# Optimization experiments

Measured on AMD Instinct MI355X. Metric: run time of the kernel, lower is better.

The kernel has to match this reference:

```python
import jax, jax.numpy as jnp
import numpy as np

N_NODES = 100_000
N_EDGES = 1_600_000
N_GRAPHS = 512
D_NODE = 128
H = 128
L_EXTRA = 2  # model_layer - 1


def _bn(x, g, b, eps=1e-5):
    # BatchNorm1d, training-mode math (biased batch variance), eval dropout = identity
    mu = jnp.mean(x, axis=0)
    var = jnp.var(x, axis=0)
    return g * (x - mu) * jax.lax.rsqrt(var + eps) + b


def _gin_conv(x, src, dst, W1, b1, bng, bnb, W2, b2):
    # GINConv (eps=0): mlp(x + sum_{j->i} x_j); mlp = Lin -> BN -> ReLU -> Lin
    agg = jax.ops.segment_sum(x[src], dst, num_segments=x.shape[0])
    h = x + agg
    h = jax.nn.relu(_bn(h @ W1 + b1, bng, bnb))
    return h @ W2 + b2


def setup_inputs():
    key = jax.random.key(0)
    ks = jax.random.split(key, 24)
    s = 0.05
    d = {}
    d["x"] = jax.random.normal(ks[0], (N_NODES, D_NODE), dtype=jnp.float32)
    d["edge_index"] = jax.random.randint(ks[1], (2, N_EDGES), 0, N_NODES, dtype=jnp.int32)
    d["batch"] = jnp.sort(jax.random.randint(ks[2], (N_NODES,), 0, N_GRAPHS, dtype=jnp.int32))
    d["vn_emb"] = jax.random.normal(ks[3], (1, H)) * s
    # conv1 MLP: Linear(D_NODE, 2H) -> BN -> ReLU -> Linear(2H, H)
    d["c1_W1"] = jax.random.normal(ks[4], (D_NODE, 2 * H)) * s
    d["c1_b1"] = jnp.zeros((2 * H,))
    d["c1_bng"] = jnp.ones((2 * H,))
    d["c1_bnb"] = jnp.zeros((2 * H,))
    d["c1_W2"] = jax.random.normal(ks[5], (2 * H, H)) * s
    d["c1_b2"] = jnp.zeros((H,))
    d["bn1_g"] = jnp.ones((H,))
    d["bn1_b"] = jnp.zeros((H,))
    # stacked extra GIN layers (model_layer - 1)
    d["cW1"] = jax.random.normal(ks[6], (L_EXTRA, H, 2 * H)) * s
    d["cb1"] = jnp.zeros((L_EXTRA, 2 * H))
    d["cbng"] = jnp.ones((L_EXTRA, 2 * H))
    d["cbnb"] = jnp.zeros((L_EXTRA, 2 * H))
    d["cW2"] = jax.random.normal(ks[7], (L_EXTRA, 2 * H, H)) * s
    d["cb2"] = jnp.zeros((L_EXTRA, H))
    d["bns_g"] = jnp.ones((L_EXTRA, H))
    d["bns_b"] = jnp.zeros((L_EXTRA, H))
    # virtual node MLP: Lin(H,2H)->BN->ReLU->Lin(2H,H)->BN->ReLU->Dropout
    d["vW1"] = jax.random.normal(ks[8], (H, 2 * H)) * s
    d["vb1"] = jnp.zeros((2 * H,))
    d["vbn1_g"] = jnp.ones((2 * H,))
    d["vbn1_b"] = jnp.zeros((2 * H,))
    d["vW2"] = jax.random.normal(ks[9], (2 * H, H)) * s
    d["vb2"] = jnp.zeros((H,))
    d["vbn2_g"] = jnp.ones((H,))
    d["vbn2_b"] = jnp.zeros((H,))
    return d


def reference(x, edge_index, batch, vn_emb, c1_W1, c1_b1, c1_bng, c1_bnb, c1_W2, c1_b2,
              bn1_g, bn1_b, cW1, cb1, cbng, cbnb, cW2, cb2, bns_g, bns_b,
              vW1, vb1, vbn1_g, vbn1_b, vW2, vb2, vbn2_g, vbn2_b):
    src, dst = edge_index[0], edge_index[1]
    # virtual node feature per graph: Embedding(1, H) indexed with zeros
    vfeat = jnp.broadcast_to(vn_emb[0], (N_GRAPHS, H))
    # layer 1: dropout is identity in eval mode
    post = jax.nn.relu(_bn(_gin_conv(x, src, dst, c1_W1, c1_b1, c1_bng, c1_bnb, c1_W2, c1_b2), bn1_g, bn1_b))
    for i in range(L_EXTRA):
        post = post + vfeat[batch]                       # virtual-node broadcast
        post = _bn(_gin_conv(post, src, dst, cW1[i], cb1[i], cbng[i], cbnb[i], cW2[i], cb2[i]), bns_g[i], bns_b[i])
        if i < L_EXTRA - 1:
            post = jax.nn.relu(post)
            pooled = jax.ops.segment_sum(post, batch, num_segments=N_GRAPHS)  # GlobalAddPool
            z = pooled + vfeat
            z = jax.nn.relu(_bn(z @ vW1 + vb1, vbn1_g, vbn1_b))
            vfeat = jax.nn.relu(_bn(z @ vW2 + vb2, vbn2_g, vbn2_b))
    # readout: global mean pool over nodes per graph
    counts = jax.ops.segment_sum(jnp.ones((x.shape[0],), post.dtype), batch, num_segments=N_GRAPHS)
    out = jax.ops.segment_sum(post, batch, num_segments=N_GRAPHS) / jnp.maximum(counts, 1.0)[:, None]
    return out
```

## Files before the change

kernel.cpp:

```cpp
#include <hip/hip_runtime.h>

#define NN 100000
#define NE 1600000
#define NG 512
#define DH 128
#define DH2 256
#define SCB 98
#define NSTRIPE 32

typedef __attribute__((ext_vector_type(8))) _Float16 h8;
typedef __attribute__((ext_vector_type(2))) _Float16 h2;
typedef __attribute__((ext_vector_type(4))) float f4;

static inline size_t align256(size_t x) { return (x + 255) & ~size_t(255); }

__global__ __launch_bounds__(256) void countslot_k(const int* __restrict__ ei,
                                                   int* __restrict__ cursor,
                                                   int* __restrict__ slot) {
    int i = blockIdx.x * blockDim.x + threadIdx.x;
    int stride = gridDim.x * blockDim.x;
    for (int e = i; e < NE; e += stride)
        slot[e] = atomicAdd(&cursor[ei[NE + e]], 1);
}

__global__ __launch_bounds__(256) void place_k(const int* __restrict__ ei,
                                               const int* __restrict__ rowptr,
                                               const int* __restrict__ slot,
                                               int* __restrict__ esrc) {
    int i = blockIdx.x * blockDim.x + threadIdx.x;
    int stride = gridDim.x * blockDim.x;
    for (int e = i; e < NE; e += stride)
        esrc[rowptr[ei[NE + e]] + slot[e]] = ei[e];
}

__global__ void gbound_k(const int* __restrict__ batch, int* __restrict__ gcnt) {
    int g = blockIdx.x * blockDim.x + threadIdx.x;
    if (g >= NG) return;
    int lo = 0, hi = NN;
    while (lo < hi) { int m = (lo + hi) >> 1; if (batch[m] < g) lo = m + 1; else hi = m; }
    int b0 = lo;
    lo = 0; hi = NN;
    int g1 = g + 1;
    while (lo < hi) { int m = (lo + hi) >> 1; if (batch[m] < g1) lo = m + 1; else hi = m; }
    gcnt[g] = lo - b0;
}

__global__ __launch_bounds__(256) void scan1_k(const int* __restrict__ deg,
                                               int* __restrict__ part) {
    int i0 = blockIdx.x * 1024 + threadIdx.x * 4;
    int s = 0;
    if (i0 < NN) {
        int4 v = *(const int4*)(deg + i0);
        s = v.x + v.y + v.z + v.w;
    }
#pragma unroll
    for (int o = 1; o < 64; o <<= 1) s += __shfl_xor(s, o);
    __shared__ int ws[4];
    if ((threadIdx.x & 63) == 0) ws[threadIdx.x >> 6] = s;
    __syncthreads();
    if (threadIdx.x == 0) part[blockIdx.x] = ws[0] + ws[1] + ws[2] + ws[3];
}

__global__ void scan2_k(int* __restrict__ part, int* __restrict__ rowptr) {
    if (threadIdx.x == 0) {
        int run = 0;
        for (int i = 0; i < SCB; i++) { int v = part[i]; part[i] = run; run += v; }
        rowptr[NN] = run;
    }
}

__global__ __launch_bounds__(256) void scan3_k(const int* __restrict__ deg,
                                               const int* __restrict__ part,
                                               int* __restrict__ rowptr) {
    int t = threadIdx.x;
    int i0 = blockIdx.x * 1024 + t * 4;
    int4 v = {0, 0, 0, 0};
    if (i0 < NN) v = *(const int4*)(deg + i0);
    int s = v.x + v.y + v.z + v.w;
    __shared__ int sc[256];
    sc[t] = s;
    __syncthreads();
    for (int o = 1; o < 256; o <<= 1) {
        int add = (t >= o) ? sc[t - o] : 0;
        __syncthreads();
        sc[t] += add;
        __syncthreads();
    }
    int excl = (t ? sc[t - 1] : 0) + part[blockIdx.x];
    if (i0 < NN) {
        int4 r;
        r.x = excl;
        r.y = excl + v.x;
        r.z = excl + v.x + v.y;
        r.w = excl + v.x + v.y + v.z;
        *(int4*)(rowptr + i0) = r;
    }
}

__global__ void castx_k(const float* __restrict__ x, _Float16* __restrict__ xh) {
    int i = blockIdx.x * blockDim.x + threadIdx.x;
    if (i >= NN * 16) return;
    const float4* s = (const float4*)x + i * 2;
    float4 p = s[0], q = s[1];
    h8 h = {(_Float16)p.x, (_Float16)p.y, (_Float16)p.z, (_Float16)p.w,
            (_Float16)q.x, (_Float16)q.y, (_Float16)q.z, (_Float16)q.w};
    ((h8*)xh)[i] = h;
}

__global__ void vinit_k(const float* __restrict__ emb, _Float16* __restrict__ vfeat) {
    int i = blockIdx.x * blockDim.x + threadIdx.x;
    if (i < NG * DH) vfeat[i] = (_Float16)emb[i & (DH - 1)];
}

__global__ void zin_k(const float* __restrict__ pooled, const _Float16* __restrict__ vf,
                      _Float16* __restrict__ zb) {
    int i = blockIdx.x * blockDim.x + threadIdx.x;
    if (i < NG * DH) zb[i] = (_Float16)(pooled[i] + (float)vf[i]);
}

__global__ void addvn_k(_Float16* __restrict__ x, const _Float16* __restrict__ vfeat,
                        const int* __restrict__ batch) {
    int i = blockIdx.x * blockDim.x + threadIdx.x;
    if (i >= NN * 16) return;
    int row = i >> 4;
    int bg = batch[row];
    h8 u = ((h8*)x)[i];
    h8 v = ((const h8*)vfeat)[bg * 16 + (i & 15)];
    h8 o;
#pragma unroll
    for (int e = 0; e < 8; e++) o[e] = (_Float16)((float)u[e] + (float)v[e]);
    ((h8*)x)[i] = o;
}

__global__ void finalout_k(const float* __restrict__ pooled2, const int* __restrict__ gcnt,
                           float* __restrict__ outp) {
    int i = blockIdx.x * blockDim.x + threadIdx.x;
    if (i >= NG * DH) return;
    float cnt = (float)gcnt[i >> 7];
    outp[i] = pooled2[i] / fmaxf(cnt, 1.0f);
}

__global__ void bnfin_k(const float* __restrict__ csum, const float* __restrict__ csq,
                        const float* __restrict__ g, const float* __restrict__ b,
                        float* __restrict__ scale, float* __restrict__ shift,
                        int NC, int M) {
    int col = threadIdx.x;
    if (col >= NC) return;
    float s = 0.f, q = 0.f;
    for (int st = 0; st < NSTRIPE; st++) { s += csum[st * NC + col]; q += csq[st * NC + col]; }
    float invM = 1.0f / (float)M;
    float mean = s * invM;
    float var = q * invM - mean * mean;
    float sc = g[col] * rsqrtf(var + 1e-5f);
    scale[col] = sc;
    shift[col] = b[col] - mean * sc;
}

struct WPack {
    const float* w[8];
    _Float16* wt[8];
    int K[8];
    int N[8];
};
__global__ void wtrans_k(WPack p) {
    int id = blockIdx.z;
    const float* W = p.w[id];
    _Float16* Wt = p.wt[id];
    int K = p.K[id], N = p.N[id];
    int n0 = blockIdx.x * 32, k0 = blockIdx.y * 32;
    if (n0 >= N || k0 >= K) return;
    __shared__ float t[32][33];
    int tx = threadIdx.x & 31, ty = threadIdx.x >> 5;
    for (int i = 0; i < 32; i += 8)
        t[ty + i][tx] = W[(size_t)(k0 + ty + i) * N + n0 + tx];
    __syncthreads();
    for (int i = 0; i < 32; i += 8)
        Wt[(size_t)(n0 + ty + i) * K + k0 + tx] = (_Float16)t[tx][ty + i];
}

__global__ __launch_bounds__(256) void agg_k(const _Float16* __restrict__ xin,
                                             const int* __restrict__ rowptr,
                                             const int* __restrict__ esrc,
                                             _Float16* __restrict__ out) {
    int wave = threadIdx.x >> 6, lane = threadIdx.x & 63;
    int node = blockIdx.x * 4 + wave;
    if (node >= NN) return;
    const h2* xr = (const h2*)xin;
    h2 self = xr[(size_t)node * 64 + lane];
    float a0 = (float)self.x, a1 = (float)self.y;
    int beg = rowptr[node], end = rowptr[node + 1];
    int j = beg;
    for (; j + 7 < end; j += 8) {
        int s0 = esrc[j],     s1 = esrc[j + 1], s2 = esrc[j + 2], s3 = esrc[j + 3];
        int s4 = esrc[j + 4], s5 = esrc[j + 5], s6 = esrc[j + 6], s7 = esrc[j + 7];
        h2 u0 = xr[(size_t)s0 * 64 + lane];
        h2 u1 = xr[(size_t)s1 * 64 + lane];
        h2 u2 = xr[(size_t)s2 * 64 + lane];
        h2 u3 = xr[(size_t)s3 * 64 + lane];
        h2 u4 = xr[(size_t)s4 * 64 + lane];
        h2 u5 = xr[(size_t)s5 * 64 + lane];
        h2 u6 = xr[(size_t)s6 * 64 + lane];
        h2 u7 = xr[(size_t)s7 * 64 + lane];
        a0 += ((float)u0.x + (float)u1.x) + ((float)u2.x + (float)u3.x)
            + ((float)u4.x + (float)u5.x) + ((float)u6.x + (float)u7.x);
        a1 += ((float)u0.y + (float)u1.y) + ((float)u2.y + (float)u3.y)
            + ((float)u4.y + (float)u5.y) + ((float)u6.y + (float)u7.y);
    }
    for (; j < end; j++) {
        h2 u = xr[(size_t)esrc[j] * 64 + lane];
        a0 += (float)u.x; a1 += (float)u.y;
    }
    h2 o; o.x = (_Float16)a0; o.y = (_Float16)a1;
    ((h2*)out)[(size_t)node * 64 + lane] = o;
}

template <int K, int NCF>
__global__ __launch_bounds__(256, 2) void mgemm_k(
        const _Float16* __restrict__ A, const _Float16* __restrict__ Wt,
        const float* __restrict__ bias, _Float16* __restrict__ C,
        float* __restrict__ csum, float* __restrict__ csq, int M,
        const float* __restrict__ bnsc, const float* __restrict__ bnsh) {
    constexpr int BK = 128;
    constexpr int LDA = BK + 8;
    __shared__ __align__(16) _Float16 As[128 * LDA];
    const int tid = threadIdx.x;
    const int lane = tid & 63;
    const int wave = tid >> 6;
    const int wr = wave & 1, wc = wave >> 1;
    const int lm = lane & 15, lq = lane >> 4;
    const int mB = blockIdx.x * 128;
    const int n0 = blockIdx.y * 128 + wc * 64;

    f4 acc[4][4];
#pragma unroll
    for (int i = 0; i < 4; i++)
#pragma unroll
        for (int j = 0; j < 4; j++) acc[i][j] = (f4){0.f, 0.f, 0.f, 0.f};

    const int sr = tid >> 4;
    const int sc = (tid & 15) * 8;

    for (int kc = 0; kc < K; kc += BK) {
        if (kc) __syncthreads();
        float bscv[8], bshv[8];
        if (bnsc) {
            float4 s0 = *(const float4*)&bnsc[kc + sc];
            float4 s1 = *(const float4*)&bnsc[kc + sc + 4];
            float4 t0 = *(const float4*)&bnsh[kc + sc];
            float4 t1 = *(const float4*)&bnsh[kc + sc + 4];
            bscv[0] = s0.x; bscv[1] = s0.y; bscv[2] = s0.z; bscv[3] = s0.w;
            bscv[4] = s1.x; bscv[5] = s1.y; bscv[6] = s1.z; bscv[7] = s1.w;
            bshv[0] = t0.x; bshv[1] = t0.y; bshv[2] = t0.z; bshv[3] = t0.w;
            bshv[4] = t1.x; bshv[5] = t1.y; bshv[6] = t1.z; bshv[7] = t1.w;
        }
#pragma unroll
        for (int rr = 0; rr < 128; rr += 16) {
            int gr = mB + rr + sr; if (gr >= M) gr = M - 1;
            h8 h = *(const h8*)&A[(size_t)gr * K + kc + sc];
            if (bnsc) {
#pragma unroll
                for (int e = 0; e < 8; e++)
                    h[e] = (_Float16)fmaxf((float)h[e] * bscv[e] + bshv[e], 0.f);
            }
            *(h8*)&As[(rr + sr) * LDA + sc] = h;
        }
        __syncthreads();
#pragma unroll
        for (int ks = 0; ks < BK / 32; ks++) {
            h8 af[4], bf[4];
#pragma unroll
            for (int t = 0; t < 4; t++) {
                af[t] = *(const h8*)&As[(wr * 64 + t * 16 + lm) * LDA + ks * 32 + lq * 8];
                bf[t] = *(const h8*)&Wt[(size_t)(n0 + t * 16 + lm) * K + kc + ks * 32 + lq * 8];
            }
#pragma unroll
            for (int i = 0; i < 4; i++)
#pragma unroll
                for (int j = 0; j < 4; j++)
                    acc[i][j] = __builtin_amdgcn_mfma_f32_16x16x32_f16(af[i], bf[j], acc[i][j], 0, 0, 0);
        }
    }

    float bv[4];
#pragma unroll
    for (int j = 0; j < 4; j++) bv[j] = bias[n0 + j * 16 + lm];
    float ls[4] = {0, 0, 0, 0}, lsq[4] = {0, 0, 0, 0};
    __syncthreads();
    _Float16* Cs = As;
#pragma unroll
    for (int i = 0; i < 4; i++) {
        int row = wr * 64 + i * 16 + lq * 4;
        bool rv[4];
#pragma unroll
        for (int r = 0; r < 4; r++) rv[r] = (mB + row + r) < M;
#pragma unroll
        for (int j = 0; j < 4; j++) {
#pragma unroll
            for (int r = 0; r < 4; r++) {
                float v = acc[i][j][r] + bv[j];
                Cs[(row + r) * LDA + wc * 64 + j * 16 + lm] = (_Float16)v;
                if (rv[r]) { ls[j] += v; lsq[j] += v * v; }
            }
        }
    }
    const int stripe = blockIdx.x & (NSTRIPE - 1);
#pragma unroll
    for (int j = 0; j < 4; j++) {
        float s = ls[j], q = lsq[j];
        s += __shfl_xor(s, 16); s += __shfl_xor(s, 32);
        q += __shfl_xor(q, 16); q += __shfl_xor(q, 32);
        if (lq == 0) {
            atomicAdd(&csum[stripe * NCF + n0 + j * 16 + lm], s);
            atomicAdd(&csq[stripe * NCF + n0 + j * 16 + lm], q);
        }
    }
    __syncthreads();
    const int trow = tid >> 4;
    const int tcol = (tid & 15) * 8;
    const int cb = blockIdx.y * 128;
#pragma unroll
    for (int p = 0; p < 8; p++) {
        int row = p * 16 + trow;
        int grow = mB + row;
        if (grow < M) {
            h8 v = *(const h8*)&Cs[row * LDA + tcol];
            *(h8*)&C[(size_t)grow * NCF + cb + tcol] = v;
        }
    }
}

__global__ void bnrelu_k(const _Float16* __restrict__ in, _Float16* __restrict__ out,
                         const float* __restrict__ scale, const float* __restrict__ shift,
                         const _Float16* __restrict__ vfeat, const int* __restrict__ batch,
                         int M) {
    constexpr int PER = 16;
    int tid = blockIdx.x * blockDim.x + threadIdx.x;
    int c8 = tid % PER;
    int c0 = c8 * 8;
    float sc[8], sh[8];
    float4 s0 = *(const float4*)&scale[c0];
    float4 s1 = *(const float4*)&scale[c0 + 4];
    float4 t0 = *(const float4*)&shift[c0];
    float4 t1 = *(const float4*)&shift[c0 + 4];
    sc[0] = s0.x; sc[1] = s0.y; sc[2] = s0.z; sc[3] = s0.w;
    sc[4] = s1.x; sc[5] = s1.y; sc[6] = s1.z; sc[7] = s1.w;
    sh[0] = t0.x; sh[1] = t0.y; sh[2] = t0.z; sh[3] = t0.w;
    sh[4] = t1.x; sh[5] = t1.y; sh[6] = t1.z; sh[7] = t1.w;
    int total = M * PER;
    int stride = gridDim.x * blockDim.x;
    for (int i = tid; i < total; i += stride) {
        int row = i / PER;
        h8 u = ((const h8*)in)[i];
        h8 w;
        bool vn = (vfeat != nullptr);
        if (vn) w = ((const h8*)vfeat)[batch[row] * PER + c8];
        h8 o;
#pragma unroll
        for (int e = 0; e < 8; e++) {
            float vv = fmaxf((float)u[e] * sc[e] + sh[e], 0.f);
            if (vn) vv += (float)w[e];
            o[e] = (_Float16)vv;
        }
        ((h8*)out)[i] = o;
    }
}

__global__ __launch_bounds__(256) void bnpool_k(
        const _Float16* __restrict__ in, _Float16* __restrict__ out,
        const float* __restrict__ scale, const float* __restrict__ shift,
        const int* __restrict__ batch, float* __restrict__ pooled,
        int M, int relu) {
    int t = threadIdx.x;
    int c0 = (t & 63) * 2;
    int r0 = blockIdx.x * 128 + (t >> 6) * 32;
    float sc0 = scale[c0], h0 = shift[c0];
    float sc1 = scale[c0 + 1], h1 = shift[c0 + 1];
    int rend = r0 + 32; if (rend > M) rend = M;
    float a0 = 0.f, a1 = 0.f; int cur = -1;
    int r = r0;
    for (; r + 1 < rend; r += 2) {
        h2 ua = ((const h2*)in)[(size_t)r * 64 + (c0 >> 1)];
        h2 ub = ((const h2*)in)[(size_t)(r + 1) * 64 + (c0 >> 1)];
        int bga = batch[r], bgb = batch[r + 1];
        float va0 = (float)ua.x * sc0 + h0, va1 = (float)ua.y * sc1 + h1;
        float vb0 = (float)ub.x * sc0 + h0, vb1 = (float)ub.y * sc1 + h1;
        if (relu) {
            va0 = fmaxf(va0, 0.f); va1 = fmaxf(va1, 0.f);
            vb0 = fmaxf(vb0, 0.f); vb1 = fmaxf(vb1, 0.f);
        }
        if (out) {
            h2 oa; oa.x = (_Float16)va0; oa.y = (_Float16)va1;
            h2 ob; ob.x = (_Float16)vb0; ob.y = (_Float16)vb1;
            ((h2*)out)[(size_t)r * 64 + (c0 >> 1)] = oa;
            ((h2*)out)[(size_t)(r + 1) * 64 + (c0 >> 1)] = ob;
        }
        if (bga != cur) {
            if (cur >= 0) {
                atomicAdd(&pooled[(size_t)cur * DH + c0], a0);
                atomicAdd(&pooled[(size_t)cur * DH + c0 + 1], a1);
            }
            cur = bga; a0 = 0.f; a1 = 0.f;
        }
        a0 += va0; a1 += va1;
        if (bgb != cur) {
            atomicAdd(&pooled[(size_t)cur * DH + c0], a0);
            atomicAdd(&pooled[(size_t)cur * DH + c0 + 1], a1);
            cur = bgb; a0 = 0.f; a1 = 0.f;
        }
        a0 += vb0; a1 += vb1;
    }
    for (; r < rend; r++) {
        h2 u = ((const h2*)in)[(size_t)r * 64 + (c0 >> 1)];
        float v0 = (float)u.x * sc0 + h0;
        float v1 = (float)u.y * sc1 + h1;
        if (relu) { v0 = fmaxf(v0, 0.f); v1 = fmaxf(v1, 0.f); }
        if (out) { h2 o; o.x = (_Float16)v0; o.y = (_Float16)v1; ((h2*)out)[(size_t)r * 64 + (c0 >> 1)] = o; }
        int bg = batch[r];
        if (bg != cur) {
            if (cur >= 0) {
                atomicAdd(&pooled[(size_t)cur * DH + c0], a0);
                atomicAdd(&pooled[(size_t)cur * DH + c0 + 1], a1);
            }
            cur = bg; a0 = 0.f; a1 = 0.f;
        }
        a0 += v0; a1 += v1;
    }
    if (cur >= 0) {
        atomicAdd(&pooled[(size_t)cur * DH + c0], a0);
        atomicAdd(&pooled[(size_t)cur * DH + c0 + 1], a1);
    }
}

extern "C" void kernel_launch(void* const* d_in, const int* in_sizes, int n_in,
                              void* d_out, int out_size, void* d_ws, size_t ws_size,
                              hipStream_t stream) {
    const float* x      = (const float*)d_in[0];
    const int*   ei     = (const int*)d_in[1];
    const int*   batch  = (const int*)d_in[2];
    const float* vn_emb = (const float*)d_in[3];
    const float* c1_W1  = (const float*)d_in[4];
    const float* c1_b1  = (const float*)d_in[5];
    const float* c1_bng = (const float*)d_in[6];
    const float* c1_bnb = (const float*)d_in[7];
    const float* c1_W2  = (const float*)d_in[8];
    const float* c1_b2  = (const float*)d_in[9];
    const float* bn1_g  = (const float*)d_in[10];
    const float* bn1_b  = (const float*)d_in[11];
    const float* cW1    = (const float*)d_in[12];
    const float* cb1    = (const float*)d_in[13];
    const float* cbng   = (const float*)d_in[14];
    const float* cbnb   = (const float*)d_in[15];
    const float* cW2    = (const float*)d_in[16];
    const float* cb2    = (const float*)d_in[17];
    const float* bns_g  = (const float*)d_in[18];
    const float* bns_b  = (const float*)d_in[19];
    const float* vW1    = (const float*)d_in[20];
    const float* vb1    = (const float*)d_in[21];
    const float* vbn1_g = (const float*)d_in[22];
    const float* vbn1_b = (const float*)d_in[23];
    const float* vW2    = (const float*)d_in[24];
    const float* vb2    = (const float*)d_in[25];
    const float* vbn2_g = (const float*)d_in[26];
    const float* vbn2_b = (const float*)d_in[27];
    float* outp = (float*)d_out;
    (void)in_sizes; (void)n_in; (void)out_size; (void)ws_size;

    char* w = (char*)d_ws;
    size_t off = 0;
    auto carve = [&](size_t bytes) -> void* {
        void* p = w + off; off = align256(off + bytes); return p;
    };
    int*   cursor  = (int*)carve((size_t)NN * 4);
    float* pooled  = (float*)carve((size_t)NG * DH * 4);
    float* pooled2 = (float*)carve((size_t)NG * DH * 4);
    float *sA[3], *qA[3], *sB[3], *qB[3], *sV1, *qV1, *sV2, *qV2;
    for (int i = 0; i < 3; i++) {
        sA[i] = (float*)carve((size_t)NSTRIPE * 256 * 4);
        qA[i] = (float*)carve((size_t)NSTRIPE * 256 * 4);
    }
    for (int i = 0; i < 3; i++) {
        sB[i] = (float*)carve((size_t)NSTRIPE * 128 * 4);
        qB[i] = (float*)carve((size_t)NSTRIPE * 128 * 4);
    }
    sV1 = (float*)carve((size_t)NSTRIPE * 256 * 4);
    qV1 = (float*)carve((size_t)NSTRIPE * 256 * 4);
    sV2 = (float*)carve((size_t)NSTRIPE * 128 * 4);
    qV2 = (float*)carve((size_t)NSTRIPE * 128 * 4);
    size_t zbytes = off;
    float *scA[3], *shA[3], *scB[3], *shB[3];
    for (int i = 0; i < 3; i++) { scA[i] = (float*)carve(256 * 4); shA[i] = (float*)carve(256 * 4); }
    for (int i = 0; i < 3; i++) { scB[i] = (float*)carve(128 * 4); shB[i] = (float*)carve(128 * 4); }
    float* scV1 = (float*)carve(256 * 4); float* shV1 = (float*)carve(256 * 4);
    float* scV2 = (float*)carve(128 * 4); float* shV2 = (float*)carve(128 * 4);
    int*   gcnt    = (int*)carve((size_t)NG * 4);
    int*   rowptr  = (int*)carve((size_t)(NN + 1) * 4);
    int*   slot    = (int*)carve((size_t)NE * 4);
    int*   esrc    = (int*)carve((size_t)NE * 4);
    int*   part    = (int*)carve((size_t)SCB * 4);
    _Float16* vfeat = (_Float16*)carve((size_t)NG * DH * 2);
    _Float16* zin   = (_Float16*)carve((size_t)NG * DH * 2);
    _Float16* zb    = (_Float16*)carve((size_t)NG * DH2 * 2);
    _Float16* vraw  = (_Float16*)carve((size_t)NG * DH * 2);
    _Float16* xh    = (_Float16*)carve((size_t)NN * DH * 2);
    _Float16* hb    = (_Float16*)carve((size_t)NN * DH * 2);
    _Float16* b1    = (_Float16*)carve((size_t)NN * DH2 * 2);
    _Float16* abuf  = (_Float16*)carve((size_t)NN * DH * 2);
    _Float16* Wt[8];
    for (int i = 0; i < 8; i++) Wt[i] = (_Float16*)carve((size_t)DH * DH2 * 2);

    WPack wp;
    wp.w[0] = c1_W1;            wp.K[0] = 128; wp.N[0] = 256;
    wp.w[1] = c1_W2;            wp.K[1] = 256; wp.N[1] = 128;
    wp.w[2] = cW1;              wp.K[2] = 128; wp.N[2] = 256;
    wp.w[3] = cW2;              wp.K[3] = 256; wp.N[3] = 128;
    wp.w[4] = cW1 + 128 * 256;  wp.K[4] = 128; wp.N[4] = 256;
    wp.w[5] = cW2 + 256 * 128;  wp.K[5] = 256; wp.N[5] = 128;
    wp.w[6] = vW1;              wp.K[6] = 128; wp.N[6] = 256;
    wp.w[7] = vW2;              wp.K[7] = 256; wp.N[7] = 128;
    for (int i = 0; i < 8; i++) wp.wt[i] = Wt[i];

    const int GB = (NN + 127) / 128;
    dim3 gemmA(GB, 2), gemmB(GB, 1);
    const float* NUL = nullptr;

    hipMemsetAsync(d_ws, 0, zbytes, stream);
    countslot_k<<<782, 256, 0, stream>>>(ei, cursor, slot);
    scan1_k<<<SCB, 256, 0, stream>>>(cursor, part);
    scan2_k<<<1, 64, 0, stream>>>(part, rowptr);
    scan3_k<<<SCB, 256, 0, stream>>>(cursor, part, rowptr);
    place_k<<<782, 256, 0, stream>>>(ei, rowptr, slot, esrc);
    gbound_k<<<2, 256, 0, stream>>>(batch, gcnt);
    wtrans_k<<<dim3(8, 8, 8), 256, 0, stream>>>(wp);
    vinit_k<<<(NG * DH + 255) / 256, 256, 0, stream>>>(vn_emb, vfeat);
    castx_k<<<(NN * 16 + 255) / 256, 256, 0, stream>>>(x, xh);

    agg_k<<<NN / 4, 256, 0, stream>>>(xh, rowptr, esrc, hb);
    mgemm_k<128, 256><<<gemmA, 256, 0, stream>>>(hb, Wt[0], c1_b1, b1, sA[0], qA[0], NN, NUL, NUL);
    bnfin_k<<<1, 256, 0, stream>>>(sA[0], qA[0], c1_bng, c1_bnb, scA[0], shA[0], 256, NN);
    mgemm_k<256, 128><<<gemmB, 256, 0, stream>>>(b1, Wt[1], c1_b2, abuf, sB[0], qB[0], NN,
                                                 scA[0], shA[0]);
    bnfin_k<<<1, 256, 0, stream>>>(sB[0], qB[0], bn1_g, bn1_b, scB[0], shB[0], 128, NN);
    bnrelu_k<<<2048, 256, 0, stream>>>(abuf, abuf, scB[0], shB[0], vfeat, batch, NN);

    agg_k<<<NN / 4, 256, 0, stream>>>(abuf, rowptr, esrc, hb);
    mgemm_k<128, 256><<<gemmA, 256, 0, stream>>>(hb, Wt[2], cb1, b1, sA[1], qA[1], NN, NUL, NUL);
    bnfin_k<<<1, 256, 0, stream>>>(sA[1], qA[1], cbng, cbnb, scA[1], shA[1], 256, NN);
    mgemm_k<256, 128><<<gemmB, 256, 0, stream>>>(b1, Wt[3], cb2, abuf, sB[1], qB[1], NN,
                                                 scA[1], shA[1]);
    bnfin_k<<<1, 256, 0, stream>>>(sB[1], qB[1], bns_g, bns_b, scB[1], shB[1], 128, NN);
    bnpool_k<<<GB, 256, 0, stream>>>(abuf, abuf, scB[1], shB[1], batch, pooled, NN, 1);

    zin_k<<<(NG * DH + 255) / 256, 256, 0, stream>>>(pooled, vfeat, zin);
    mgemm_k<128, 256><<<dim3(4, 2), 256, 0, stream>>>(zin, Wt[6], vb1, zb, sV1, qV1, NG, NUL, NUL);
    bnfin_k<<<1, 256, 0, stream>>>(sV1, qV1, vbn1_g, vbn1_b, scV1, shV1, 256, NG);
    mgemm_k<256, 128><<<dim3(4, 1), 256, 0, stream>>>(zb, Wt[7], vb2, vraw, sV2, qV2, NG,
                                                      scV1, shV1);
    bnfin_k<<<1, 256, 0, stream>>>(sV2, qV2, vbn2_g, vbn2_b, scV2, shV2, 128, NG);
    bnrelu_k<<<32, 256, 0, stream>>>(vraw, vfeat, scV2, shV2, nullptr, nullptr, NG);

    addvn_k<<<(NN * 16 + 255) / 256, 256, 0, stream>>>(abuf, vfeat, batch);
    agg_k<<<NN / 4, 256, 0, stream>>>(abuf, rowptr, esrc, hb);
    mgemm_k<128, 256><<<gemmA, 256, 0, stream>>>(hb, Wt[4], cb1 + 256, b1, sA[2], qA[2], NN, NUL, NUL);
    bnfin_k<<<1, 256, 0, stream>>>(sA[2], qA[2], cbng + 256, cbnb + 256, scA[2], shA[2], 256, NN);
    mgemm_k<256, 128><<<gemmB, 256, 0, stream>>>(b1, Wt[5], cb2 + 128, abuf, sB[2], qB[2], NN,
                                                 scA[2], shA[2]);
    bnfin_k<<<1, 256, 0, stream>>>(sB[2], qB[2], bns_g + 128, bns_b + 128, scB[2], shB[2], 128, NN);
    bnpool_k<<<GB, 256, 0, stream>>>(abuf, nullptr, scB[2], shB[2], batch, pooled2, NN, 0);

    finalout_k<<<(NG * DH + 255) / 256, 256, 0, stream>>>(pooled2, gcnt, outp);
}
```

Baseline: 812.6 us.

## Fuse BN/ReLU and virtual-node add into aggregation gather; merge prep kernels

Merges the cast, edge-count, virtual-node init and graph-boundary kernels into one prep launch. Removes the standalone BN+ReLU+vnode pass, the addvn pass and the normalized-output writes in bnpool. Instead, the aggregation kernel applies the BN scale/shift, ReLU and virtual-node add on the fly to each gathered neighbour row. This drops several full passes over the 100k×128 activations, but each edge now costs an extra batch-index lookup, an extra vfeat gather and more ALU work.

Result: slower. 836.5 us (+2.9%).

```diff
diff --git a/kernel.cpp b/kernel.cpp
--- a/kernel.cpp
+++ b/kernel.cpp
@@ -14,13 +14,38 @@
 
 static inline size_t align256(size_t x) { return (x + 255) & ~size_t(255); }
 
-__global__ __launch_bounds__(256) void countslot_k(const int* __restrict__ ei,
-                                                   int* __restrict__ cursor,
-                                                   int* __restrict__ slot) {
-    int i = blockIdx.x * blockDim.x + threadIdx.x;
-    int stride = gridDim.x * blockDim.x;
-    for (int e = i; e < NE; e += stride)
+#define PRE_CAST (NN * 16)
+#define PRE_EDGE (PRE_CAST + NE)
+#define PRE_VIN  (PRE_EDGE + NG * DH)
+#define PRE_GB   (PRE_VIN + NG)
+__global__ __launch_bounds__(256) void prep_k(
+        const float* __restrict__ x, _Float16* __restrict__ xh,
+        const int* __restrict__ ei, int* __restrict__ cursor, int* __restrict__ slot,
+        const float* __restrict__ emb, _Float16* __restrict__ vfeat,
+        const int* __restrict__ batch, int* __restrict__ gcnt) {
+    int gid = blockIdx.x * 256 + threadIdx.x;
+    if (gid < PRE_CAST) {
+        const float4* s = (const float4*)x + gid * 2;
+        float4 p = s[0], q = s[1];
+        h8 h = {(_Float16)p.x, (_Float16)p.y, (_Float16)p.z, (_Float16)p.w,
+                (_Float16)q.x, (_Float16)q.y, (_Float16)q.z, (_Float16)q.w};
+        ((h8*)xh)[gid] = h;
+    } else if (gid < PRE_EDGE) {
+        int e = gid - PRE_CAST;
         slot[e] = atomicAdd(&cursor[ei[NE + e]], 1);
+    } else if (gid < PRE_VIN) {
+        int i = gid - PRE_EDGE;
+        vfeat[i] = (_Float16)emb[i & (DH - 1)];
+    } else if (gid < PRE_GB) {
+        int g = gid - PRE_VIN;
+        int lo = 0, hi = NN;
+        while (lo < hi) { int m = (lo + hi) >> 1; if (batch[m] < g) lo = m + 1; else hi = m; }
+        int b0 = lo;
+        lo = 0; hi = NN;
+        int g1 = g + 1;
+        while (lo < hi) { int m = (lo + hi) >> 1; if (batch[m] < g1) lo = m + 1; else hi = m; }
+        gcnt[g] = lo - b0;
+    }
 }
 
 __global__ __launch_bounds__(256) void place_k(const int* __restrict__ ei,
@@ -31,18 +56,6 @@
     int stride = gridDim.x * blockDim.x;
     for (int e = i; e < NE; e += stride)
         esrc[rowptr[ei[NE + e]] + slot[e]] = ei[e];
-}
-
-__global__ void gbound_k(const int* __restrict__ batch, int* __restrict__ gcnt) {
-    int g = blockIdx.x * blockDim.x + threadIdx.x;
-    if (g >= NG) return;
-    int lo = 0, hi = NN;
-    while (lo < hi) { int m = (lo + hi) >> 1; if (batch[m] < g) lo = m + 1; else hi = m; }
-    int b0 = lo;
-    lo = 0; hi = NN;
-    int g1 = g + 1;
-    while (lo < hi) { int m = (lo + hi) >> 1; if (batch[m] < g1) lo = m + 1; else hi = m; }
-    gcnt[g] = lo - b0;
 }
 
 __global__ __launch_bounds__(256) void scan1_k(const int* __restrict__ deg,
@@ -97,39 +110,10 @@
     }
 }
 
-__global__ void castx_k(const float* __restrict__ x, _Float16* __restrict__ xh) {
-    int i = blockIdx.x * blockDim.x + threadIdx.x;
-    if (i >= NN * 16) return;
-    const float4* s = (const float4*)x + i * 2;
-    float4 p = s[0], q = s[1];
-    h8 h = {(_Float16)p.x, (_Float16)p.y, (_Float16)p.z, (_Float16)p.w,
-            (_Float16)q.x, (_Float16)q.y, (_Float16)q.z, (_Float16)q.w};
-    ((h8*)xh)[i] = h;
-}
-
-__global__ void vinit_k(const float* __restrict__ emb, _Float16* __restrict__ vfeat) {
-    int i = blockIdx.x * blockDim.x + threadIdx.x;
-    if (i < NG * DH) vfeat[i] = (_Float16)emb[i & (DH - 1)];
-}
-
 __global__ void zin_k(const float* __restrict__ pooled, const _Float16* __restrict__ vf,
                       _Float16* __restrict__ zb) {
     int i = blockIdx.x * blockDim.x + threadIdx.x;
     if (i < NG * DH) zb[i] = (_Float16)(pooled[i] + (float)vf[i]);
-}
-
-__global__ void addvn_k(_Float16* __restrict__ x, const _Float16* __restrict__ vfeat,
-                        const int* __restrict__ batch) {
-    int i = blockIdx.x * blockDim.x + threadIdx.x;
-    if (i >= NN * 16) return;
-    int row = i >> 4;
-    int bg = batch[row];
-    h8 u = ((h8*)x)[i];
-    h8 v = ((const h8*)vfeat)[bg * 16 + (i & 15)];
-    h8 o;
-#pragma unroll
-    for (int e = 0; e < 8; e++) o[e] = (_Float16)((float)u[e] + (float)v[e]);
-    ((h8*)x)[i] = o;
 }
 
 __global__ void finalout_k(const float* __restrict__ pooled2, const int* __restrict__ gcnt,
@@ -214,6 +198,60 @@
     ((h2*)out)[(size_t)node * 64 + lane] = o;
 }
 
+__global__ __launch_bounds__(256) void aggbn_k(const _Float16* __restrict__ xin,
+                                               const int* __restrict__ rowptr,
+                                               const int* __restrict__ esrc,
+                                               const float* __restrict__ scale,
+                                               const float* __restrict__ shift,
+                                               const _Float16* __restrict__ vfeat,
+                                               const int* __restrict__ batch,
+                                               _Float16* __restrict__ out) {
+    int wave = threadIdx.x >> 6, lane = threadIdx.x & 63;
+    int node = blockIdx.x * 4 + wave;
+    if (node >= NN) return;
+    int c0 = lane * 2;
+    float sc0 = scale[c0], sh0 = shift[c0];
+    float sc1 = scale[c0 + 1], sh1 = shift[c0 + 1];
+    const h2* xr = (const h2*)xin;
+    const h2* vf = (const h2*)vfeat;
+    h2 su = xr[(size_t)node * 64 + lane];
+    h2 sw = vf[(size_t)batch[node] * 64 + lane];
+    float a0 = fmaxf((float)su.x * sc0 + sh0, 0.f) + (float)sw.x;
+    float a1 = fmaxf((float)su.y * sc1 + sh1, 0.f) + (float)sw.y;
+    int beg = rowptr[node], end = rowptr[node + 1];
+    int j = beg;
+    for (; j + 3 < end; j += 4) {
+        int s0 = esrc[j], s1 = esrc[j + 1], s2 = esrc[j + 2], s3 = esrc[j + 3];
+        int g0 = batch[s0], g1 = batch[s1], g2 = batch[s2], g3 = batch[s3];
+        h2 u0 = xr[(size_t)s0 * 64 + lane];
+        h2 u1 = xr[(size_t)s1 * 64 + lane];
+        h2 u2 = xr[(size_t)s2 * 64 + lane];
+        h2 u3 = xr[(size_t)s3 * 64 + lane];
+        h2 w0 = vf[(size_t)g0 * 64 + lane];
+        h2 w1 = vf[(size_t)g1 * 64 + lane];
+        h2 w2 = vf[(size_t)g2 * 64 + lane];
+        h2 w3 = vf[(size_t)g3 * 64 + lane];
+        a0 += fmaxf((float)u0.x * sc0 + sh0, 0.f) + (float)w0.x
+            + fmaxf((float)u1.x * sc0 + sh0, 0.f) + (float)w1.x
+            + fmaxf((float)u2.x * sc0 + sh0, 0.f) + (float)w2.x
+            + fmaxf((float)u3.x * sc0 + sh0, 0.f) + (float)w3.x;
+        a1 += fmaxf((float)u0.y * sc1 + sh1, 0.f) + (float)w0.y
+            + fmaxf((float)u1.y * sc1 + sh1, 0.f) + (float)w1.y
+            + fmaxf((float)u2.y * sc1 + sh1, 0.f) + (float)w2.y
+            + fmaxf((float)u3.y * sc1 + sh1, 0.f) + (float)w3.y;
+    }
+    for (; j < end; j++) {
+        int s = esrc[j];
+        int g = batch[s];
+        h2 u = xr[(size_t)s * 64 + lane];
+        h2 w = vf[(size_t)g * 64 + lane];
+        a0 += fmaxf((float)u.x * sc0 + sh0, 0.f) + (float)w.x;
+        a1 += fmaxf((float)u.y * sc1 + sh1, 0.f) + (float)w.y;
+    }
+    h2 o; o.x = (_Float16)a0; o.y = (_Float16)a1;
+    ((h2*)out)[(size_t)node * 64 + lane] = o;
+}
+
 template <int K, int NCF>
 __global__ __launch_bounds__(256, 2) void mgemm_k(
         const _Float16* __restrict__ A, const _Float16* __restrict__ Wt,
@@ -331,7 +369,6 @@
 
 __global__ void bnrelu_k(const _Float16* __restrict__ in, _Float16* __restrict__ out,
                          const float* __restrict__ scale, const float* __restrict__ shift,
-                         const _Float16* __restrict__ vfeat, const int* __restrict__ batch,
                          int M) {
     constexpr int PER = 16;
     int tid = blockIdx.x * blockDim.x + threadIdx.x;
@@ -349,24 +386,17 @@
     int total = M * PER;
     int stride = gridDim.x * blockDim.x;
     for (int i = tid; i < total; i += stride) {
-        int row = i / PER;
         h8 u = ((const h8*)in)[i];
-        h8 w;
-        bool vn = (vfeat != nullptr);
-        if (vn) w = ((const h8*)vfeat)[batch[row] * PER + c8];
         h8 o;
 #pragma unroll
-        for (int e = 0; e < 8; e++) {
-            float vv = fmaxf((float)u[e] * sc[e] + sh[e], 0.f);
-            if (vn) vv += (float)w[e];
-            o[e] = (_Float16)vv;
-        }
+        for (int e = 0; e < 8; e++)
+            o[e] = (_Float16)fmaxf((float)u[e] * sc[e] + sh[e], 0.f);
         ((h8*)out)[i] = o;
     }
 }
 
 __global__ __launch_bounds__(256) void bnpool_k(
-        const _Float16* __restrict__ in, _Float16* __restrict__ out,
+        const _Float16* __restrict__ in,
         const float* __restrict__ scale, const float* __restrict__ shift,
         const int* __restrict__ batch, float* __restrict__ pooled,
         int M, int relu) {
@@ -388,12 +418,6 @@
             va0 = fmaxf(va0, 0.f); va1 = fmaxf(va1, 0.f);
             vb0 = fmaxf(vb0, 0.f); vb1 = fmaxf(vb1, 0.f);
         }
-        if (out) {
-            h2 oa; oa.x = (_Float16)va0; oa.y = (_Float16)va1;
-            h2 ob; ob.x = (_Float16)vb0; ob.y = (_Float16)vb1;
-            ((h2*)out)[(size_t)r * 64 + (c0 >> 1)] = oa;
-            ((h2*)out)[(size_t)(r + 1) * 64 + (c0 >> 1)] = ob;
-        }
         if (bga != cur) {
             if (cur >= 0) {
                 atomicAdd(&pooled[(size_t)cur * DH + c0], a0);
@@ -414,7 +438,6 @@
         float v0 = (float)u.x * sc0 + h0;
         float v1 = (float)u.y * sc1 + h1;
         if (relu) { v0 = fmaxf(v0, 0.f); v1 = fmaxf(v1, 0.f); }
-        if (out) { h2 o; o.x = (_Float16)v0; o.y = (_Float16)v1; ((h2*)out)[(size_t)r * 64 + (c0 >> 1)] = o; }
         int bg = batch[r];
         if (bg != cur) {
             if (cur >= 0) {
@@ -522,17 +545,15 @@
     const int GB = (NN + 127) / 128;
     dim3 gemmA(GB, 2), gemmB(GB, 1);
     const float* NUL = nullptr;
+    const int PREP_BLOCKS = (PRE_GB + 255) / 256;
 
     hipMemsetAsync(d_ws, 0, zbytes, stream);
-    countslot_k<<<782, 256, 0, stream>>>(ei, cursor, slot);
+    prep_k<<<PREP_BLOCKS, 256, 0, stream>>>(x, xh, ei, cursor, slot, vn_emb, vfeat, batch, gcnt);
     scan1_k<<<SCB, 256, 0, stream>>>(cursor, part);
     scan2_k<<<1, 64, 0, stream>>>(part, rowptr);
     scan3_k<<<SCB, 256, 0, stream>>>(cursor, part, rowptr);
     place_k<<<782, 256, 0, stream>>>(ei, rowptr, slot, esrc);
-    gbound_k<<<2, 256, 0, stream>>>(batch, gcnt);
     wtrans_k<<<dim3(8, 8, 8), 256, 0, stream>>>(wp);
-    vinit_k<<<(NG * DH + 255) / 256, 256, 0, stream>>>(vn_emb, vfeat);
-    castx_k<<<(NN * 16 + 255) / 256, 256, 0, stream>>>(x, xh);
 
     agg_k<<<NN / 4, 256, 0, stream>>>(xh, rowptr, esrc, hb);
     mgemm_k<128, 256><<<gemmA, 256, 0, stream>>>(hb, Wt[0], c1_b1, b1, sA[0], qA[0], NN, NUL, NUL);
@@ -540,15 +561,14 @@
     mgemm_k<256, 128><<<gemmB, 256, 0, stream>>>(b1, Wt[1], c1_b2, abuf, sB[0], qB[0], NN,
                                                  scA[0], shA[0]);
     bnfin_k<<<1, 256, 0, stream>>>(sB[0], qB[0], bn1_g, bn1_b, scB[0], shB[0], 128, NN);
-    bnrelu_k<<<2048, 256, 0, stream>>>(abuf, abuf, scB[0], shB[0], vfeat, batch, NN);
-
-    agg_k<<<NN / 4, 256, 0, stream>>>(abuf, rowptr, esrc, hb);
+
+    aggbn_k<<<NN / 4, 256, 0, stream>>>(abuf, rowptr, esrc, scB[0], shB[0], vfeat, batch, hb);
     mgemm_k<128, 256><<<gemmA, 256, 0, stream>>>(hb, Wt[2], cb1, b1, sA[1], qA[1], NN, NUL, NUL);
     bnfin_k<<<1, 256, 0, stream>>>(sA[1], qA[1], cbng, cbnb, scA[1], shA[1], 256, NN);
     mgemm_k<256, 128><<<gemmB, 256, 0, stream>>>(b1, Wt[3], cb2, abuf, sB[1], qB[1], NN,
                                                  scA[1], shA[1]);
     bnfin_k<<<1, 256, 0, stream>>>(sB[1], qB[1], bns_g, bns_b, scB[1], shB[1], 128, NN);
-    bnpool_k<<<GB, 256, 0, stream>>>(abuf, abuf, scB[1], shB[1], batch, pooled, NN, 1);
+    bnpool_k<<<GB, 256, 0, stream>>>(abuf, scB[1], shB[1], batch, pooled, NN, 1);
 
     zin_k<<<(NG * DH + 255) / 256, 256, 0, stream>>>(pooled, vfeat, zin);
     mgemm_k<128, 256><<<dim3(4, 2), 256, 0, stream>>>(zin, Wt[6], vb1, zb, sV1, qV1, NG, NUL, NUL);
@@ -556,16 +576,15 @@
     mgemm_k<256, 128><<<dim3(4, 1), 256, 0, stream>>>(zb, Wt[7], vb2, vraw, sV2, qV2, NG,
                                                       scV1, shV1);
     bnfin_k<<<1, 256, 0, stream>>>(sV2, qV2, vbn2_g, vbn2_b, scV2, shV2, 128, NG);
-    bnrelu_k<<<32, 256, 0, stream>>>(vraw, vfeat, scV2, shV2, nullptr, nullptr, NG);
-
-    addvn_k<<<(NN * 16 + 255) / 256, 256, 0, stream>>>(abuf, vfeat, batch);
-    agg_k<<<NN / 4, 256, 0, stream>>>(abuf, rowptr, esrc, hb);
+    bnrelu_k<<<32, 256, 0, stream>>>(vraw, vfeat, scV2, shV2, NG);
+
+    aggbn_k<<<NN / 4, 256, 0, stream>>>(abuf, rowptr, esrc, scB[1], shB[1], vfeat, batch, hb);
     mgemm_k<128, 256><<<gemmA, 256, 0, stream>>>(hb, Wt[4], cb1 + 256, b1, sA[2], qA[2], NN, NUL, NUL);
     bnfin_k<<<1, 256, 0, stream>>>(sA[2], qA[2], cbng + 256, cbnb + 256, scA[2], shA[2], 256, NN);
     mgemm_k<256, 128><<<gemmB, 256, 0, stream>>>(b1, Wt[5], cb2 + 128, abuf, sB[2], qB[2], NN,
                                                  scA[2], shA[2]);
     bnfin_k<<<1, 256, 0, stream>>>(sB[2], qB[2], bns_g + 128, bns_b + 128, scB[2], shB[2], 128, NN);
-    bnpool_k<<<GB, 256, 0, stream>>>(abuf, nullptr, scB[2], shB[2], batch, pooled2, NN, 0);
+    bnpool_k<<<GB, 256, 0, stream>>>(abuf, scB[2], shB[2], batch, pooled2, NN, 0);
 
     finalout_k<<<(NG * DH + 255) / 256, 256, 0, stream>>>(pooled2, gcnt, outp);
 }
```

## Fuse BN finalize into GEMM tails and compute all 256 columns per block

Applied to the files above, without the earlier changes.

Removes the separate single-block bnfin_k launches. Each GEMM now counts finished blocks with an atomic counter, and the last block computes the BatchNorm scale and shift. The first-layer GEMM also computes both 128-column halves in one block, so the A tile is loaded once instead of once per grid column. This doubles the accumulator registers and adds a threadfence plus an atomic per block. It also relies on the done counters being zeroed by the workspace memset, which needs the new counter to sit inside the zeroed range.

Result: slower. 1.325 ms (+63.1%).

```diff
diff --git a/kernel.cpp b/kernel.cpp
--- a/kernel.cpp
+++ b/kernel.cpp
@@ -138,22 +138,6 @@
     if (i >= NG * DH) return;
     float cnt = (float)gcnt[i >> 7];
     outp[i] = pooled2[i] / fmaxf(cnt, 1.0f);
-}
-
-__global__ void bnfin_k(const float* __restrict__ csum, const float* __restrict__ csq,
-                        const float* __restrict__ g, const float* __restrict__ b,
-                        float* __restrict__ scale, float* __restrict__ shift,
-                        int NC, int M) {
-    int col = threadIdx.x;
-    if (col >= NC) return;
-    float s = 0.f, q = 0.f;
-    for (int st = 0; st < NSTRIPE; st++) { s += csum[st * NC + col]; q += csq[st * NC + col]; }
-    float invM = 1.0f / (float)M;
-    float mean = s * invM;
-    float var = q * invM - mean * mean;
-    float sc = g[col] * rsqrtf(var + 1e-5f);
-    scale[col] = sc;
-    shift[col] = b[col] - mean * sc;
 }
 
 struct WPack {
@@ -214,13 +198,144 @@
     ((h2*)out)[(size_t)node * 64 + lane] = o;
 }
 
-template <int K, int NCF>
-__global__ __launch_bounds__(256, 2) void mgemm_k(
+__device__ __forceinline__ void bnfin_tail(
+        float* __restrict__ csum, float* __restrict__ csq,
+        const float* __restrict__ g, const float* __restrict__ b,
+        float* __restrict__ scale, float* __restrict__ shift,
+        int* __restrict__ done, int nblocks, int NC, int M, int tid) {
+    __shared__ int lastflag;
+    __threadfence();
+    if (tid == 0) {
+        int v = __hip_atomic_fetch_add(done, 1, __ATOMIC_ACQ_REL, __HIP_MEMORY_SCOPE_AGENT);
+        lastflag = (v == nblocks - 1) ? 1 : 0;
+    }
+    __syncthreads();
+    if (!lastflag) return;
+    for (int col = tid; col < NC; col += 256) {
+        float s = 0.f, q = 0.f;
+        for (int st = 0; st < NSTRIPE; st++) {
+            s += __hip_atomic_load(&csum[st * NC + col], __ATOMIC_RELAXED, __HIP_MEMORY_SCOPE_AGENT);
+            q += __hip_atomic_load(&csq[st * NC + col], __ATOMIC_RELAXED, __HIP_MEMORY_SCOPE_AGENT);
+        }
+        float invM = 1.0f / (float)M;
+        float mean = s * invM;
+        float var = q * invM - mean * mean;
+        float sc = g[col] * rsqrtf(var + 1e-5f);
+        scale[col] = sc;
+        shift[col] = b[col] - mean * sc;
+    }
+}
+
+__global__ __launch_bounds__(256, 2) void gemmA_k(
         const _Float16* __restrict__ A, const _Float16* __restrict__ Wt,
         const float* __restrict__ bias, _Float16* __restrict__ C,
         float* __restrict__ csum, float* __restrict__ csq, int M,
-        const float* __restrict__ bnsc, const float* __restrict__ bnsh) {
-    constexpr int BK = 128;
+        const float* __restrict__ g, const float* __restrict__ b,
+        float* __restrict__ scale, float* __restrict__ shift,
+        int* __restrict__ done, int nblocks) {
+    constexpr int K = 128, NCF = 256;
+    constexpr int LDA = K + 8;
+    __shared__ __align__(16) _Float16 As[128 * LDA];
+    const int tid = threadIdx.x;
+    const int lane = tid & 63;
+    const int wave = tid >> 6;
+    const int wr = wave & 1, wc = wave >> 1;
+    const int lm = lane & 15, lq = lane >> 4;
+    const int mB = blockIdx.x * 128;
+
+    const int sr = tid >> 4;
+    const int sc = (tid & 15) * 8;
+#pragma unroll
+    for (int rr = 0; rr < 128; rr += 16) {
+        int gr = mB + rr + sr; if (gr >= M) gr = M - 1;
+        *(h8*)&As[(rr + sr) * LDA + sc] = *(const h8*)&A[(size_t)gr * K + sc];
+    }
+    __syncthreads();
+
+    f4 acc[4][8];
+#pragma unroll
+    for (int i = 0; i < 4; i++)
+#pragma unroll
+        for (int jj = 0; jj < 8; jj++) acc[i][jj] = (f4){0.f, 0.f, 0.f, 0.f};
+#pragma unroll
+    for (int ct = 0; ct < 2; ct++) {
+        const int n0 = ct * 128 + wc * 64;
+#pragma unroll
+        for (int ks = 0; ks < 4; ks++) {
+            h8 af[4], bf[4];
+#pragma unroll
+            for (int t = 0; t < 4; t++) {
+                af[t] = *(const h8*)&As[(wr * 64 + t * 16 + lm) * LDA + ks * 32 + lq * 8];
+                bf[t] = *(const h8*)&Wt[(size_t)(n0 + t * 16 + lm) * K + ks * 32 + lq * 8];
+            }
+#pragma unroll
+            for (int i = 0; i < 4; i++)
+#pragma unroll
+                for (int j = 0; j < 4; j++)
+                    acc[i][ct * 4 + j] =
+                        __builtin_amdgcn_mfma_f32_16x16x32_f16(af[i], bf[j], acc[i][ct * 4 + j], 0, 0, 0);
+        }
+    }
+
+    float bv[8];
+#pragma unroll
+    for (int jj = 0; jj < 8; jj++) bv[jj] = bias[(jj >> 2) * 128 + wc * 64 + (jj & 3) * 16 + lm];
+    float ls[8] = {0, 0, 0, 0, 0, 0, 0, 0}, lsq[8] = {0, 0, 0, 0, 0, 0, 0, 0};
+    _Float16* Cs = As;
+    const int trow = tid >> 4;
+    const int tcol = (tid & 15) * 8;
+#pragma unroll
+    for (int half = 0; half < 2; half++) {
+        __syncthreads();
+#pragma unroll
+        for (int i = 0; i < 4; i++) {
+            int row = wr * 64 + i * 16 + lq * 4;
+#pragma unroll
+            for (int j = 0; j < 4; j++) {
+                int jj = half * 4 + j;
+#pragma unroll
+                for (int r = 0; r < 4; r++) {
+                    float v = acc[i][jj][r] + bv[jj];
+                    Cs[(row + r) * LDA + wc * 64 + j * 16 + lm] = (_Float16)v;
+                    if (mB + row + r < M) { ls[jj] += v; lsq[jj] += v * v; }
+                }
+            }
+        }
+        __syncthreads();
+#pragma unroll
+        for (int p = 0; p < 8; p++) {
+            int row = p * 16 + trow;
+            int grow = mB + row;
+            if (grow < M) {
+                h8 v = *(const h8*)&Cs[row * LDA + tcol];
+                *(h8*)&C[(size_t)grow * NCF + half * 128 + tcol] = v;
+            }
+        }
+    }
+    const int stripe = blockIdx.x & (NSTRIPE - 1);
+#pragma unroll
+    for (int jj = 0; jj < 8; jj++) {
+        float s = ls[jj], q = lsq[jj];
+        s += __shfl_xor(s, 16); s += __shfl_xor(s, 32);
+        q += __shfl_xor(q, 16); q += __shfl_xor(q, 32);
+        if (lq == 0) {
+            int col = (jj >> 2) * 128 + wc * 64 + (jj & 3) * 16 + lm;
+            atomicAdd(&csum[stripe * NCF + col], s);
+            atomicAdd(&csq[stripe * NCF + col], q);
+        }
+    }
+    bnfin_tail(csum, csq, g, b, scale, shift, done, nblocks, NCF, M, tid);
+}
+
+__global__ __launch_bounds__(256, 2) void gemmB_k(
+        const _Float16* __restrict__ A, const _Float16* __restrict__ Wt,
+        const float* __restrict__ bias, _Float16* __restrict__ C,
+        float* __restrict__ csum, float* __restrict__ csq, int M,
+        const float* __restrict__ bnsc, const float* __restrict__ bnsh,
+        const float* __restrict__ g, const float* __restrict__ b,
+        float* __restrict__ scale, float* __restrict__ shift,
+        int* __restrict__ done, int nblocks) {
+    constexpr int K = 256, NCF = 128, BK = 128;
     constexpr int LDA = BK + 8;
     __shared__ __align__(16) _Float16 As[128 * LDA];
     const int tid = threadIdx.x;
@@ -229,7 +344,7 @@
     const int wr = wave & 1, wc = wave >> 1;
     const int lm = lane & 15, lq = lane >> 4;
     const int mB = blockIdx.x * 128;
-    const int n0 = blockIdx.y * 128 + wc * 64;
+    const int n0 = wc * 64;
 
     f4 acc[4][4];
 #pragma unroll
@@ -243,7 +358,7 @@
     for (int kc = 0; kc < K; kc += BK) {
         if (kc) __syncthreads();
         float bscv[8], bshv[8];
-        if (bnsc) {
+        {
             float4 s0 = *(const float4*)&bnsc[kc + sc];
             float4 s1 = *(const float4*)&bnsc[kc + sc + 4];
             float4 t0 = *(const float4*)&bnsh[kc + sc];
@@ -257,11 +372,9 @@
         for (int rr = 0; rr < 128; rr += 16) {
             int gr = mB + rr + sr; if (gr >= M) gr = M - 1;
             h8 h = *(const h8*)&A[(size_t)gr * K + kc + sc];
-            if (bnsc) {
-#pragma unroll
-                for (int e = 0; e < 8; e++)
-                    h[e] = (_Float16)fmaxf((float)h[e] * bscv[e] + bshv[e], 0.f);
-            }
+#pragma unroll
+            for (int e = 0; e < 8; e++)
+                h[e] = (_Float16)fmaxf((float)h[e] * bscv[e] + bshv[e], 0.f);
             *(h8*)&As[(rr + sr) * LDA + sc] = h;
         }
         __syncthreads();
@@ -317,16 +430,16 @@
     __syncthreads();
     const int trow = tid >> 4;
     const int tcol = (tid & 15) * 8;
-    const int cb = blockIdx.y * 128;
 #pragma unroll
     for (int p = 0; p < 8; p++) {
         int row = p * 16 + trow;
         int grow = mB + row;
         if (grow < M) {
             h8 v = *(const h8*)&Cs[row * LDA + tcol];
-            *(h8*)&C[(size_t)grow * NCF + cb + tcol] = v;
-        }
-    }
+            *(h8*)&C[(size_t)grow * NCF + tcol] = v;
+        }
+    }
+    bnfin_tail(csum, csq, g, b, scale, shift, done, nblocks, NCF, M, tid);
 }
 
 __global__ void bnrelu_k(const _Float16* __restrict__ in, _Float16* __restrict__ out,
@@ -473,6 +586,7 @@
     int*   cursor  = (int*)carve((size_t)NN * 4);
     float* pooled  = (float*)carve((size_t)NG * DH * 4);
     float* pooled2 = (float*)carve((size_t)NG * DH * 4);
+    int*   done    = (int*)carve(8 * 4);
     float *sA[3], *qA[3], *sB[3], *qB[3], *sV1, *qV1, *sV2, *qV2;
     for (int i = 0; i < 3; i++) {
         sA[i] = (float*)carve((size_t)NSTRIPE * 256 * 4);
@@ -520,8 +634,6 @@
     for (int i = 0; i < 8; i++) wp.wt[i] = Wt[i];
 
     const int GB = (NN + 127) / 128;
-    dim3 gemmA(GB, 2), gemmB(GB, 1);
-    const float* NUL = nullptr;
 
     hipMemsetAsync(d_ws, 0, zbytes, stream);
     countslot_k<<<782, 256, 0, stream>>>(ei, cursor, slot);
@@ -535,36 +647,33 @@
     castx_k<<<(NN * 16 + 255) / 256, 256, 0, stream>>>(x, xh);
 
     agg_k<<<NN / 4, 256, 0, stream>>>(xh, rowptr, esrc, hb);
-    mgemm_k<128, 256><<<gemmA, 256, 0, stream>>>(hb, Wt[0], c1_b1, b1, sA[0], qA[0], NN, NUL, NUL);
-    bnfin_k<<<1, 256, 0, stream>>>(sA[0], qA[0], c1_bng, c1_bnb, scA[0], shA[0], 256, NN);
-    mgemm_k<256, 128><<<gemmB, 256, 0, stream>>>(b1, Wt[1], c1_b2, abuf, sB[0], qB[0], NN,
-                                                 scA[0], shA[0]);
-    bnfin_k<<<1, 256, 0, stream>>>(sB[0], qB[0], bn1_g, bn1_b, scB[0], shB[0], 128, NN);
+    gemmA_k<<<GB, 256, 0, stream>>>(hb, Wt[0], c1_b1, b1, sA[0], qA[0], NN,
+                                    c1_bng, c1_bnb, scA[0], shA[0], &done[0], GB);
+    gemmB_k<<<GB, 256, 0, stream>>>(b1, Wt[1], c1_b2, abuf, sB[0], qB[0], NN,
+                                    scA[0], shA[0], bn1_g, bn1_b, scB[0], shB[0], &done[1], GB);
     bnrelu_k<<<2048, 256, 0, stream>>>(abuf, abuf, scB[0], shB[0], vfeat, batch, NN);
 
     agg_k<<<NN / 4, 256, 0, stream>>>(abuf, rowptr, esrc, hb);
-    mgemm_k<128, 256><<<gemmA, 256, 0, stream>>>(hb, Wt[2], cb1, b1, sA[1], qA[1], NN, NUL, NUL);
-    bnfin_k<<<1, 256, 0, stream>>>(sA[1], qA[1], cbng, cbnb, scA[1], shA[1], 256, NN);
-    mgemm_k<256, 128><<<gemmB, 256, 0, stream>>>(b1, Wt[3], cb2, abuf, sB[1], qB[1], NN,
-                                                 scA[1], shA[1]);
-    bnfin_k<<<1, 256, 0, stream>>>(sB[1], qB[1], bns_g, bns_b, scB[1], shB[1], 128, NN);
+    gemmA_k<<<GB, 256, 0, stream>>>(hb, Wt[2], cb1, b1, sA[1], qA[1], NN,
+                                    cbng, cbnb, scA[1], shA[1], &done[2], GB);
+    gemmB_k<<<GB, 256, 0, stream>>>(b1, Wt[3], cb2, abuf, sB[1], qB[1], NN,
+                                    scA[1], shA[1], bns_g, bns_b, scB[1], shB[1], &done[3], GB);
     bnpool_k<<<GB, 256, 0, stream>>>(abuf, abuf, scB[1], shB[1], batch, pooled, NN, 1);
 
     zin_k<<<(NG * DH + 255) / 256, 256, 0, stream>>>(pooled, vfeat, zin);
-    mgemm_k<128, 256><<<dim3(4, 2), 256, 0, stream>>>(zin, Wt[6], vb1, zb, sV1, qV1, NG, NUL, NUL);
-    bnfin_k<<<1, 256, 0, stream>>>(sV1, qV1, vbn1_g, vbn1_b, scV1, shV1, 256, NG);
-    mgemm_k<256, 128><<<dim3(4, 1), 256, 0, stream>>>(zb, Wt[7], vb2, vraw, sV2, qV2, NG,
-                                                      scV1, shV1);
-    bnfin_k<<<1, 256, 0, stream>>>(sV2, qV2, vbn2_g, vbn2_b, scV2, shV2, 128, NG);
+    gemmA_k<<<4, 256, 0, stream>>>(zin, Wt[6], vb1, zb, sV1, qV1, NG,
+                                   vbn1_g, vbn1_b, scV1, shV1, &done[6], 4);
+    gemmB_k<<<4, 256, 0, stream>>>(zb, Wt[7], vb2, vraw, sV2, qV2, NG,
+                                   scV1, shV1, vbn2_g, vbn2_b, scV2, shV2, &done[7], 4);
     bnrelu_k<<<32, 256, 0, stream>>>(vraw, vfeat, scV2, shV2, nullptr, nullptr, NG);
 
     addvn_k<<<(NN * 16 + 255) / 256, 256, 0, stream>>>(abuf, vfeat, batch);
     agg_k<<<NN / 4, 256, 0, stream>>>(abuf, rowptr, esrc, hb);
-    mgemm_k<128, 256><<<gemmA, 256, 0, stream>>>(hb, Wt[4], cb1 + 256, b1, sA[2], qA[2], NN, NUL, NUL);
-    bnfin_k<<<1, 256, 0, stream>>>(sA[2], qA[2], cbng + 256, cbnb + 256, scA[2], shA[2], 256, NN);
-    mgemm_k<256, 128><<<gemmB, 256, 0, stream>>>(b1, Wt[5], cb2 + 128, abuf, sB[2], qB[2], NN,
-                                                 scA[2], shA[2]);
-    bnfin_k<<<1, 256, 0, stream>>>(sB[2], qB[2], bns_g + 128, bns_b + 128, scB[2], shB[2], 128, NN);
+    gemmA_k<<<GB, 256, 0, stream>>>(hb, Wt[4], cb1 + 256, b1, sA[2], qA[2], NN,
+                                    cbng + 256, cbnb + 256, scA[2], shA[2], &done[4], GB);
+    gemmB_k<<<GB, 256, 0, stream>>>(b1, Wt[5], cb2 + 128, abuf, sB[2], qB[2], NN,
+                                    scA[2], shA[2], bns_g + 128, bns_b + 128, scB[2], shB[2],
+                                    &done[5], GB);
     bnpool_k<<<GB, 256, 0, stream>>>(abuf, nullptr, scB[2], shB[2], batch, pooled2, NN, 0);
 
     finalout_k<<<(NG * DH + 255) / 256, 256, 0, stream>>>(pooled2, gcnt, outp);
```
